# Kernel tuning notes

Measured on AMD Instinct MI355X. Metric: run time of the kernel, lower is better.

## Reference

```python
import jax, jax.numpy as jnp
import numpy as np

N_NODES = 10000
IN_CH = 128
OUT_CH = 128
N_EDGES = 320000


def setup_inputs() -> dict:
    key = jax.random.key(0)
    k1, k2, k3, k4 = jax.random.split(key, 4)
    x = jax.random.normal(k1, (N_NODES, IN_CH), dtype=jnp.float32)
    edge_index = jax.random.randint(k2, (N_EDGES, 2), 0, N_NODES, dtype=jnp.int64)
    # Linear weights (torch stores [out, in]); scale like kaiming-uniform-ish
    w = jax.random.normal(k3, (OUT_CH, IN_CH), dtype=jnp.float32) / np.sqrt(IN_CH)
    b = jax.random.normal(k4, (OUT_CH, IN_CH), dtype=jnp.float32) / np.sqrt(IN_CH)
    return {"x": x, "edge_index": edge_index, "w": w, "b": b}


def reference(x, edge_index, w, b):
    n = x.shape[0]
    # Each edge (i, j) contributes x[j] to node i and x[i] to node j (undirected).
    src = jnp.concatenate([edge_index[:, 1], edge_index[:, 0]])  # feature source
    dst = jnp.concatenate([edge_index[:, 0], edge_index[:, 1]])  # aggregation target
    # segment-sum of gathered neighbor features -> [n, in_ch]
    agg_sum = jax.ops.segment_sum(x[src], dst, num_segments=n)
    deg = jax.ops.segment_sum(jnp.ones_like(dst, dtype=x.dtype), dst, num_segments=n)
    # mean with zero fallback for isolated nodes (original uses zeros vector)
    agg = jnp.where(deg[:, None] > 0, agg_sum / jnp.maximum(deg, 1.0)[:, None], 0.0)
    # out = ReLU(agg @ w^T + x @ b^T)
    return jax.nn.relu(agg @ w.T + x @ b.T)
```

## Files before the change

kernel.cpp:

```cpp
#include <hip/hip_runtime.h>

#define N_NODES 10000
#define CH 128
#define N_EDGES 320000
#define CAP 128
#define CSTR 16

#define NSLICE 8
#define FILL_CHUNKS (N_EDGES / 256)
#define FILL_BLOCKS (FILL_CHUNKS * NSLICE)
#define CONV_THREADS (N_NODES * CH / 8)
#define CONV_BLOCKS ((CONV_THREADS + 255) / 256)
#define PACK_THREADS (128 * 128)
#define PACK_BLOCKS (PACK_THREADS / 256)
#define KSEG 5
#define WBK (KSEG * CH)
#define NPB2 16
#define AP 136


typedef __attribute__((ext_vector_type(8))) short short8v;
typedef __attribute__((ext_vector_type(4))) float floatx4;

__device__ __forceinline__ unsigned short f2bf(float f) {
    unsigned u = __float_as_uint(f);
    return (unsigned short)((u + 0x7FFFu + ((u >> 16) & 1u)) >> 16);
}
__device__ __forceinline__ float bf2f(unsigned short h) {
    return __uint_as_float(((unsigned)h) << 16);
}

__global__ __launch_bounds__(256) void fill_conv_pack_kernel(const int* __restrict__ ei,
                                                             int* __restrict__ cursor,
                                                             unsigned short* __restrict__ adj,
                                                             const float* __restrict__ x,
                                                             unsigned short* __restrict__ xhi,
                                                             unsigned short* __restrict__ xlo,
                                                             const float* __restrict__ w,
                                                             const float* __restrict__ b,
                                                             unsigned short* __restrict__ wbt)
{
    const int bid = blockIdx.x;
    if (bid < CONV_BLOCKS) {
        const int t = bid * 256 + threadIdx.x;
        const float4 a = ((const float4*)x)[t * 2];
        const float4 c = ((const float4*)x)[t * 2 + 1];
        ushort4 h0, h1, l0, l1;
        h0.x = f2bf(a.x); l0.x = f2bf(a.x - bf2f(h0.x));
        h0.y = f2bf(a.y); l0.y = f2bf(a.y - bf2f(h0.y));
        h0.z = f2bf(a.z); l0.z = f2bf(a.z - bf2f(h0.z));
        h0.w = f2bf(a.w); l0.w = f2bf(a.w - bf2f(h0.w));
        h1.x = f2bf(c.x); l1.x = f2bf(c.x - bf2f(h1.x));
        h1.y = f2bf(c.y); l1.y = f2bf(c.y - bf2f(h1.y));
        h1.z = f2bf(c.z); l1.z = f2bf(c.z - bf2f(h1.z));
        h1.w = f2bf(c.w); l1.w = f2bf(c.w - bf2f(h1.w));
        ((ushort4*)xhi)[t * 2]     = h0;
        ((ushort4*)xhi)[t * 2 + 1] = h1;
        ((ushort4*)xlo)[t * 2]     = l0;
        ((ushort4*)xlo)[t * 2 + 1] = l1;
    } else if (bid < CONV_BLOCKS + FILL_BLOCKS) {
        const int fb    = bid - CONV_BLOCKS;
        const int slice = fb & (NSLICE - 1);
        const int chunk = fb >> 3;
        const int t = chunk * 256 + threadIdx.x;
        const int2 p = ((const int2*)ei)[t];
        const int a = p.x, c = p.y;
        const bool aok = (unsigned)a < N_NODES && (unsigned)c < N_NODES;
        if (aok && (a & 7) == slice) {
            const int s0 = atomicAdd(&cursor[a * CSTR], 1);
            if (s0 < CAP) adj[(size_t)a * CAP + s0] = (unsigned short)c;
        }
        if (aok && (c & 7) == slice) {
            const int s1 = atomicAdd(&cursor[c * CSTR], 1);
            if (s1 < CAP) adj[(size_t)c * CAP + s1] = (unsigned short)a;
        }
    } else {
        const int t = (bid - CONV_BLOCKS - FILL_BLOCKS) * 256 + threadIdx.x;
        const int n = t >> 7;
        const int k = t & 127;
        const float wv = w[n * CH + k];
        const float bv = b[n * CH + k];
        const unsigned short whi = f2bf(wv);
        const unsigned short wlo = f2bf(wv - bf2f(whi));
        const unsigned short bhi = f2bf(bv);
        const unsigned short blo = f2bf(bv - bf2f(bhi));
        unsigned short* row = wbt + (size_t)n * WBK;
        row[k]          = whi;
        row[CH + k]     = wlo;
        row[2 * CH + k] = bhi;
        row[3 * CH + k] = blo;
        row[4 * CH + k] = bhi;
    }
}

__global__ __launch_bounds__(512) void gather_mfma_kernel(const unsigned short* __restrict__ xhi,
                                                          const unsigned short* __restrict__ xlo,
                                                          const int* __restrict__ cursor,
                                                          const unsigned short* __restrict__ adj,
                                                          const unsigned short* __restrict__ wbt,
                                                          float* __restrict__ out)
{
    __shared__ unsigned short sh_a[NPB2 * AP];
    const int tid   = threadIdx.x;
    const int wv    = tid >> 6;
    const int lane  = tid & 63;
    const int node0 = blockIdx.x * NPB2;

    const int h = lane >> 4;
    const int l = lane & 15;

#pragma unroll
    for (int i = 0; i < 2; ++i) {
        const int nl   = wv * 2 + i;
        const int node = node0 + nl;
        const int deg  = cursor[node * CSTR];
        const int d    = deg < CAP ? deg : CAP;
        const unsigned short* nb = adj + (size_t)node * CAP;

        float4 accA = {0.f, 0.f, 0.f, 0.f};
        float4 accB = {0.f, 0.f, 0.f, 0.f};
        const int nit = (d + 3) >> 2;
#pragma unroll 4
        for (int it = 0; it < nit; ++it) {
            const int idx = 4 * it + h;
            int j = nb[idx];
            j = j < N_NODES ? j : 0;
            const uint4 q = ((const uint4*)(xhi + (size_t)j * CH))[l];
            const float m = idx < d ? 1.0f : 0.0f;
            accA.x += m * __uint_as_float(q.x << 16);
            accA.y += m * __uint_as_float(q.x & 0xffff0000u);
            accA.z += m * __uint_as_float(q.y << 16);
            accA.w += m * __uint_as_float(q.y & 0xffff0000u);
            accB.x += m * __uint_as_float(q.z << 16);
            accB.y += m * __uint_as_float(q.z & 0xffff0000u);
            accB.z += m * __uint_as_float(q.w << 16);
            accB.w += m * __uint_as_float(q.w & 0xffff0000u);
        }
        accA.x += __shfl_xor(accA.x, 16, 64);
        accA.y += __shfl_xor(accA.y, 16, 64);
        accA.z += __shfl_xor(accA.z, 16, 64);
        accA.w += __shfl_xor(accA.w, 16, 64);
        accB.x += __shfl_xor(accB.x, 16, 64);
        accB.y += __shfl_xor(accB.y, 16, 64);
        accB.z += __shfl_xor(accB.z, 16, 64);
        accB.w += __shfl_xor(accB.w, 16, 64);
        accA.x += __shfl_xor(accA.x, 32, 64);
        accA.y += __shfl_xor(accA.y, 32, 64);
        accA.z += __shfl_xor(accA.z, 32, 64);
        accA.w += __shfl_xor(accA.w, 32, 64);
        accB.x += __shfl_xor(accB.x, 32, 64);
        accB.y += __shfl_xor(accB.y, 32, 64);
        accB.z += __shfl_xor(accB.z, 32, 64);
        accB.w += __shfl_xor(accB.w, 32, 64);

        if (h == 0) {
            const float inv = deg > 0 ? 1.0f / (float)deg : 0.0f;
            uint4 o;
            o.x = (unsigned)f2bf(accA.x * inv) | ((unsigned)f2bf(accA.y * inv) << 16);
            o.y = (unsigned)f2bf(accA.z * inv) | ((unsigned)f2bf(accA.w * inv) << 16);
            o.z = (unsigned)f2bf(accB.x * inv) | ((unsigned)f2bf(accB.y * inv) << 16);
            o.w = (unsigned)f2bf(accB.z * inv) | ((unsigned)f2bf(accB.w * inv) << 16);
            ((uint4*)(sh_a + (size_t)nl * AP))[l] = o;
        }
    }
    __syncthreads();

    const int r  = lane & 15;
    const int q  = lane >> 4;
    const int n0 = wv * 16;
    const unsigned short* brow = wbt + (size_t)(n0 + r) * WBK;
    floatx4 acc = {0.f, 0.f, 0.f, 0.f};

#pragma unroll
    for (int seg = 0; seg < KSEG; ++seg) {
        const int wk = seg * CH;
#pragma unroll
        for (int ks = 0; ks < 4; ++ks) {
            const int k0 = ks * 32 + q * 8;
            short8v af;
            if (seg < 2) {
                af = *(const short8v*)(sh_a + (size_t)r * AP + k0);
            } else if (seg < 4) {
                af = *(const short8v*)(xhi + (size_t)(node0 + r) * CH + k0);
            } else {
                af = *(const short8v*)(xlo + (size_t)(node0 + r) * CH + k0);
            }
            const short8v bf = *(const short8v*)(brow + wk + k0);
            acc = __builtin_amdgcn_mfma_f32_16x16x32_bf16(af, bf, acc, 0, 0, 0);
        }
    }

    const int mbase = node0 + q * 4;
#pragma unroll
    for (int rr = 0; rr < 4; ++rr) {
        float v = acc[rr];
        v = v > 0.f ? v : 0.f;
        out[(size_t)(mbase + rr) * CH + n0 + r] = v;
    }
}

extern "C" void kernel_launch(void* const* d_in, const int* in_sizes, int n_in,
                              void* d_out, int out_size, void* d_ws, size_t ws_size,
                              hipStream_t stream)
{
    const float* x  = (const float*)d_in[0];
    const int*   ei = (const int*)d_in[1];
    const float* w  = (const float*)d_in[2];
    const float* b  = (const float*)d_in[3];
    float*       out = (float*)d_out;

    int*            cursor = (int*)d_ws;
    unsigned short* adj    = (unsigned short*)((char*)d_ws + 640000);
    unsigned short* xhi    = (unsigned short*)((char*)d_ws + 3200000);
    unsigned short* xlo    = (unsigned short*)((char*)d_ws + 5760000);
    unsigned short* wbt    = (unsigned short*)((char*)d_ws + 8320000);

    hipMemsetAsync(d_ws, 0, (size_t)N_NODES * CSTR * sizeof(int), stream);

    fill_conv_pack_kernel<<<CONV_BLOCKS + FILL_BLOCKS + PACK_BLOCKS, 256, 0, stream>>>(
        ei, cursor, adj, x, xhi, xlo, w, b, wbt);
    gather_mfma_kernel<<<N_NODES / NPB2, 512, 0, stream>>>(xhi, xlo, cursor, adj, wbt, out);
}
```

Baseline: 124.9 us.

## Split per-node adjacency into four sub-lists to cut atomic contention

Each node's adjacency list becomes four sub-lists of capacity 48, each with its own cursor counter, and edges are assigned to a sub-list by edge index. This spreads atomics on hot nodes across four addresses. Fill blocks now handle two edge chunks each and are ordered before the conversion blocks. In the gather, each quarter-wave walks its own sub-list, masked against the longest one, which adds idle iterations when sub-list lengths differ. The per-sub-list capacity cap could drop edges on high-degree nodes, unlike the old cap of 128 per node.

```diff
diff --git a/kernel.cpp b/kernel.cpp
--- a/kernel.cpp
+++ b/kernel.cpp
@@ -3,11 +3,13 @@
 #define N_NODES 10000
 #define CH 128
 #define N_EDGES 320000
-#define CAP 128
 #define CSTR 16
+#define NSUB 4
+#define SUBCAP 48
+#define ADJSTR (NSUB * SUBCAP)
 
 #define NSLICE 8
-#define FILL_CHUNKS (N_EDGES / 256)
+#define FILL_CHUNKS (N_EDGES / 512)
 #define FILL_BLOCKS (FILL_CHUNKS * NSLICE)
 #define CONV_THREADS (N_NODES * CH / 8)
 #define CONV_BLOCKS ((CONV_THREADS + 255) / 256)
@@ -41,8 +43,27 @@
                                                              unsigned short* __restrict__ wbt)
 {
     const int bid = blockIdx.x;
-    if (bid < CONV_BLOCKS) {
-        const int t = bid * 256 + threadIdx.x;
+    if (bid < FILL_BLOCKS) {
+        const int slice = bid & (NSLICE - 1);
+        const int chunk = bid >> 3;
+#pragma unroll
+        for (int e = 0; e < 2; ++e) {
+            const int t = chunk * 512 + e * 256 + threadIdx.x;
+            const int2 p = ((const int2*)ei)[t];
+            const int a = p.x, c = p.y;
+            if ((unsigned)a >= N_NODES || (unsigned)c >= N_NODES) continue;
+            const int sub = t & 3;
+            if ((a & 7) == slice) {
+                const int s0 = atomicAdd(&cursor[a * CSTR + sub], 1);
+                if (s0 < SUBCAP) adj[(size_t)a * ADJSTR + sub * SUBCAP + s0] = (unsigned short)c;
+            }
+            if ((c & 7) == slice) {
+                const int s1 = atomicAdd(&cursor[c * CSTR + sub], 1);
+                if (s1 < SUBCAP) adj[(size_t)c * ADJSTR + sub * SUBCAP + s1] = (unsigned short)a;
+            }
+        }
+    } else if (bid < FILL_BLOCKS + CONV_BLOCKS) {
+        const int t = (bid - FILL_BLOCKS) * 256 + threadIdx.x;
         const float4 a = ((const float4*)x)[t * 2];
         const float4 c = ((const float4*)x)[t * 2 + 1];
         ushort4 h0, h1, l0, l1;
@@ -58,24 +79,8 @@
         ((ushort4*)xhi)[t * 2 + 1] = h1;
         ((ushort4*)xlo)[t * 2]     = l0;
         ((ushort4*)xlo)[t * 2 + 1] = l1;
-    } else if (bid < CONV_BLOCKS + FILL_BLOCKS) {
-        const int fb    = bid - CONV_BLOCKS;
-        const int slice = fb & (NSLICE - 1);
-        const int chunk = fb >> 3;
-        const int t = chunk * 256 + threadIdx.x;
-        const int2 p = ((const int2*)ei)[t];
-        const int a = p.x, c = p.y;
-        const bool aok = (unsigned)a < N_NODES && (unsigned)c < N_NODES;
-        if (aok && (a & 7) == slice) {
-            const int s0 = atomicAdd(&cursor[a * CSTR], 1);
-            if (s0 < CAP) adj[(size_t)a * CAP + s0] = (unsigned short)c;
-        }
-        if (aok && (c & 7) == slice) {
-            const int s1 = atomicAdd(&cursor[c * CSTR], 1);
-            if (s1 < CAP) adj[(size_t)c * CAP + s1] = (unsigned short)a;
-        }
     } else {
-        const int t = (bid - CONV_BLOCKS - FILL_BLOCKS) * 256 + threadIdx.x;
+        const int t = (bid - FILL_BLOCKS - CONV_BLOCKS) * 256 + threadIdx.x;
         const int n = t >> 7;
         const int k = t & 127;
         const float wv = w[n * CH + k];
@@ -113,20 +118,26 @@
     for (int i = 0; i < 2; ++i) {
         const int nl   = wv * 2 + i;
         const int node = node0 + nl;
-        const int deg  = cursor[node * CSTR];
-        const int d    = deg < CAP ? deg : CAP;
-        const unsigned short* nb = adj + (size_t)node * CAP;
+        const int4 c4  = *((const int4*)(cursor + node * CSTR));
+        const int deg  = c4.x + c4.y + c4.z + c4.w;
+        const int d0 = c4.x < SUBCAP ? c4.x : SUBCAP;
+        const int d1 = c4.y < SUBCAP ? c4.y : SUBCAP;
+        const int d2 = c4.z < SUBCAP ? c4.z : SUBCAP;
+        const int d3 = c4.w < SUBCAP ? c4.w : SUBCAP;
+        const int cq = h == 0 ? d0 : (h == 1 ? d1 : (h == 2 ? d2 : d3));
+        const int m01 = d0 > d1 ? d0 : d1;
+        const int m23 = d2 > d3 ? d2 : d3;
+        const int nmax = m01 > m23 ? m01 : m23;
+        const unsigned short* nb = adj + (size_t)node * ADJSTR + h * SUBCAP;
 
         float4 accA = {0.f, 0.f, 0.f, 0.f};
         float4 accB = {0.f, 0.f, 0.f, 0.f};
-        const int nit = (d + 3) >> 2;
-#pragma unroll 4
-        for (int it = 0; it < nit; ++it) {
-            const int idx = 4 * it + h;
-            int j = nb[idx];
+#pragma unroll 8
+        for (int it = 0; it < nmax; ++it) {
+            int j = nb[it];
             j = j < N_NODES ? j : 0;
             const uint4 q = ((const uint4*)(xhi + (size_t)j * CH))[l];
-            const float m = idx < d ? 1.0f : 0.0f;
+            const float m = it < cq ? 1.0f : 0.0f;
             accA.x += m * __uint_as_float(q.x << 16);
             accA.y += m * __uint_as_float(q.x & 0xffff0000u);
             accA.z += m * __uint_as_float(q.y << 16);
@@ -211,13 +222,13 @@
 
     int*            cursor = (int*)d_ws;
     unsigned short* adj    = (unsigned short*)((char*)d_ws + 640000);
-    unsigned short* xhi    = (unsigned short*)((char*)d_ws + 3200000);
-    unsigned short* xlo    = (unsigned short*)((char*)d_ws + 5760000);
-    unsigned short* wbt    = (unsigned short*)((char*)d_ws + 8320000);
+    unsigned short* xhi    = (unsigned short*)((char*)d_ws + 4480000);
+    unsigned short* xlo    = (unsigned short*)((char*)d_ws + 7040000);
+    unsigned short* wbt    = (unsigned short*)((char*)d_ws + 9600000);
 
     hipMemsetAsync(d_ws, 0, (size_t)N_NODES * CSTR * sizeof(int), stream);
 
-    fill_conv_pack_kernel<<<CONV_BLOCKS + FILL_BLOCKS + PACK_BLOCKS, 256, 0, stream>>>(
+    fill_conv_pack_kernel<<<FILL_BLOCKS + CONV_BLOCKS + PACK_BLOCKS, 256, 0, stream>>>(
         ei, cursor, adj, x, xhi, xlo, w, b, wbt);
     gather_mfma_kernel<<<N_NODES / NPB2, 512, 0, stream>>>(xhi, xlo, cursor, adj, wbt, out);
 }
```

After: 131.0 us. 1.05x slower.
